# Kernel tuning notes

Measured on AMD Instinct MI355X. Metric: run time of the kernel, lower is better.

## Reference

```python
import jax, jax.numpy as jnp
import numpy as np
from jax import lax

EPS = 1e-6
CLAMP = 1e4


def _ln_last(x, w, b):
    # fp32 LayerNorm over last dim
    mu = jnp.mean(x, axis=-1, keepdims=True)
    var = jnp.mean(jnp.square(x - mu), axis=-1, keepdims=True)
    return (x - mu) * lax.rsqrt(var + EPS) * w + b


def _nan_clean(x):
    return jnp.nan_to_num(x, nan=0.0, posinf=CLAMP, neginf=-CLAMP)


def setup_inputs() -> dict:
    key = jax.random.key(0)
    B, C, H, W = 4, 256, 64, 64
    hid = 2 * C  # expand=2
    k = 3        # d_conv
    ks = jax.random.split(key, 12)
    s = 0.02
    return {
        "x": jax.random.normal(ks[0], (B, C, H, W), jnp.float32),
        "ln2d_w": jnp.ones((C,), jnp.float32),
        "ln2d_b": jnp.zeros((C,), jnp.float32),
        "inproj_w": jax.random.normal(ks[1], (C, C), jnp.float32) * s,
        "inproj_b": jnp.zeros((C,), jnp.float32),
        "dw2d_w": jax.random.normal(ks[2], (C, 3, 3), jnp.float32) * s,
        "dw2d_b": jnp.zeros((C,), jnp.float32),
        "ssm_ln_w": jnp.ones((C,), jnp.float32),
        "ssm_ln_b": jnp.zeros((C,), jnp.float32),
        "ssm_in_w": jax.random.normal(ks[3], (2 * hid, C), jnp.float32) * s,
        "ssm_in_b": jnp.zeros((2 * hid,), jnp.float32),
        "ssm_dw_w": jax.random.normal(ks[4], (hid, k), jnp.float32) * s,
        "ssm_dw_b": jnp.zeros((hid,), jnp.float32),
        "ssm_out_w": jax.random.normal(ks[5], (C, hid), jnp.float32) * s,
        "ssm_out_b": jnp.zeros((C,), jnp.float32),
        "outproj_w": jax.random.normal(ks[6], (C, C), jnp.float32) * s,
        "outproj_b": jnp.zeros((C,), jnp.float32),
    }


def reference(x, ln2d_w, ln2d_b, inproj_w, inproj_b, dw2d_w, dw2d_b,
              ssm_ln_w, ssm_ln_b, ssm_in_w, ssm_in_b, ssm_dw_w, ssm_dw_b,
              ssm_out_w, ssm_out_b, outproj_w, outproj_b):
    B, C, H, W = x.shape
    L = H * W

    # LN2d over channel dim (per-pixel LN on C)
    y = _ln_last(x.transpose(0, 2, 3, 1), ln2d_w, ln2d_b).transpose(0, 3, 1, 2)

    # 1x1 conv in_proj
    y = jnp.einsum('bchw,oc->bohw', y, inproj_w) + inproj_b[None, :, None, None]

    # depthwise 3x3 conv, SAME padding
    y = lax.conv_general_dilated(
        y, dw2d_w[:, None, :, :], (1, 1), ((1, 1), (1, 1)),
        dimension_numbers=('NCHW', 'OIHW', 'NCHW'),
        feature_group_count=C) + dw2d_b[None, :, None, None]

    # cross-scan: 4 routes (B,L,C)
    s0 = y.reshape(B, C, L).transpose(0, 2, 1)                      # row-major
    s1 = s0[:, ::-1]                                                # reversed
    s2 = y.transpose(0, 1, 3, 2).reshape(B, C, L).transpose(0, 2, 1)  # col-major
    s3 = s2[:, ::-1]
    s = jnp.concatenate([s0, s1, s2, s3], axis=0)  # (4B, L, C), shared SSM weights

    # MambaOrLite fallback: LN -> GLU -> depthwise conv1d -> out proj + residual
    r = _ln_last(s, ssm_ln_w, ssm_ln_b)
    r = r @ ssm_in_w.T + ssm_in_b                   # (4B, L, 2*hid)
    a, g = jnp.split(r, 2, axis=-1)
    r = a * jax.nn.sigmoid(g)                       # (4B, L, hid)
    r = r.transpose(0, 2, 1)                        # (4B, hid, L)
    hid = r.shape[1]
    k = ssm_dw_w.shape[-1]
    pad = ((k - 1) // 2, k // 2)
    r = lax.conv_general_dilated(
        r, ssm_dw_w[:, None, :], (1,), (pad,),
        dimension_numbers=('NCH', 'OIH', 'NCH'),
        feature_group_count=hid) + ssm_dw_b[None, :, None]
    r = r.transpose(0, 2, 1) @ ssm_out_w.T + ssm_out_b  # (4B, L, C)
    ys = _nan_clean(r) + s

    # cross-merge: average the 4 routes back to (B,C,H,W)
    y0, y1, y2, y3 = jnp.split(ys, 4, axis=0)
    m0 = y0.transpose(0, 2, 1).reshape(B, C, H, W)
    m1 = y1[:, ::-1].transpose(0, 2, 1).reshape(B, C, H, W)
    m2 = y2.transpose(0, 2, 1).reshape(B, C, W, H).transpose(0, 1, 3, 2)
    m3 = y3[:, ::-1].transpose(0, 2, 1).reshape(B, C, W, H).transpose(0, 1, 3, 2)
    m = (m0 + m1 + m2 + m3) * 0.25

    out = jnp.einsum('bchw,oc->bohw', m, outproj_w) + outproj_b[None, :, None, None]
    out = _nan_clean(out)
    return out + x
```

## Files before the change

### kernel.cpp

```cpp
#include <hip/hip_runtime.h>

typedef float f32x4 __attribute__((ext_vector_type(4)));
typedef __bf16 bf16x8 __attribute__((ext_vector_type(8)));
typedef unsigned short u16;
typedef unsigned int u32;

__device__ __forceinline__ float bf2f(u32 bits16) {
  u32 x = (bits16 & 0xffffu) << 16;
  return __builtin_bit_cast(float, x);
}
__device__ __forceinline__ u16 f2bf(float f) {
  u32 x = __builtin_bit_cast(u32, f);
  x += 0x7fffu + ((x >> 16) & 1u);
  return (u16)(x >> 16);
}
__device__ __forceinline__ void gload16(const void* g, void* l) {
  __builtin_amdgcn_global_load_lds((__attribute__((address_space(1))) void*)g,
                                   (__attribute__((address_space(3))) void*)l,
                                   16, 0, 0);
}

__global__ __launch_bounds__(256) void k_tobf16(const float* __restrict__ s,
                                                u16* __restrict__ d, int n) {
  int i = (blockIdx.x * 256 + threadIdx.x) * 4;
  if (i + 3 < n) {
    float4 v = *(const float4*)&s[i];
    u32 a = (u32)f2bf(v.x) | ((u32)f2bf(v.y) << 16);
    u32 b = (u32)f2bf(v.z) | ((u32)f2bf(v.w) << 16);
    *(uint2*)&d[i] = make_uint2(a, b);
  }
}

__global__ __launch_bounds__(256) void k_cvec(const float* __restrict__ Wout,
                                              const float* __restrict__ dwb,
                                              const float* __restrict__ outb,
                                              float* __restrict__ cvec) {
  int o = threadIdx.x;
  float s = outb[o];
  for (int k = 0; k < 512; ++k) s += dwb[k] * Wout[o * 512 + k];
  cvec[o] = s;
}

__global__ __launch_bounds__(256) void k_dwT(const float* __restrict__ dww,
                                             float* __restrict__ wT) {
  int c = threadIdx.x;
  #pragma unroll
  for (int j = 0; j < 9; ++j) wT[j * 256 + c] = dww[c * 9 + j];
}

__global__ __launch_bounds__(512) void k_scanw(const float* __restrict__ dww,
                                               float* __restrict__ w02,
                                               float* __restrict__ w14) {
  int c = threadIdx.x;
  w02[c] = dww[c * 3 + 0] + dww[c * 3 + 2];
  w14[c] = 4.f * dww[c * 3 + 1];
}

__global__ __launch_bounds__(256)
void k_ln2d(const float* __restrict__ x, const float* __restrict__ lw,
            const float* __restrict__ lb, u16* __restrict__ A) {
  __shared__ float ps1[4][64], ps2[4][64];
  __shared__ float mu[64], rsd[64];
  __shared__ float T[64 * 67];
  int tid = threadIdx.x;
  int wv = tid >> 6, p = tid & 63;
  int n0 = blockIdx.x * 64;
  int bb = n0 >> 12;
  int hw0 = n0 & 4095;
  const float* xb = x + ((size_t)bb << 20);
  float s1 = 0.f, s2 = 0.f;
  for (int i = 0; i < 64; ++i) {
    int c = wv * 64 + i;
    float v = xb[((size_t)c << 12) + hw0 + p];
    s1 += v; s2 += v * v;
  }
  ps1[wv][p] = s1; ps2[wv][p] = s2;
  __syncthreads();
  if (tid < 64) {
    float S1 = ps1[0][tid] + ps1[1][tid] + ps1[2][tid] + ps1[3][tid];
    float S2 = ps2[0][tid] + ps2[1][tid] + ps2[2][tid] + ps2[3][tid];
    float m = S1 * (1.f / 256.f);
    float var = S2 * (1.f / 256.f) - m * m;
    mu[tid] = m;
    rsd[tid] = rsqrtf(var + 1e-6f);
  }
  __syncthreads();
  for (int cc = 0; cc < 4; ++cc) {
    #pragma unroll
    for (int i = 0; i < 16; ++i) {
      int cl = i * 4 + wv;
      int c = cc * 64 + cl;
      float v = xb[((size_t)c << 12) + hw0 + p];
      T[cl * 67 + p] = (v - mu[p]) * rsd[p] * lw[c] + lb[c];
    }
    __syncthreads();
    int p2b = tid >> 4, c4 = (tid & 15) * 4;
    #pragma unroll
    for (int i2 = 0; i2 < 4; ++i2) {
      int p2 = p2b + 16 * i2;
      u32 a = (u32)f2bf(T[(c4 + 0) * 67 + p2]) | ((u32)f2bf(T[(c4 + 1) * 67 + p2]) << 16);
      u32 b = (u32)f2bf(T[(c4 + 2) * 67 + p2]) | ((u32)f2bf(T[(c4 + 3) * 67 + p2]) << 16);
      *(uint2*)&A[(size_t)(n0 + p2) * 256 + cc * 64 + c4] = make_uint2(a, b);
    }
    __syncthreads();
  }
}

__global__ __launch_bounds__(256)
void k_dw3x3_ln(const u16* __restrict__ Y1, const float* __restrict__ wT,
                const float* __restrict__ dwb, const float* __restrict__ lnw,
                const float* __restrict__ lnb, u16* __restrict__ Yc,
                u16* __restrict__ A) {
  int tid = threadIdx.x;
  int n = blockIdx.x * 4 + (tid >> 6);
  int lane = tid & 63;
  int c0 = lane * 4;
  int b = n >> 12, hw = n & 4095, h = hw >> 6, w = hw & 63;
  float4 b4 = *(const float4*)&dwb[c0];
  float a0 = b4.x, a1 = b4.y, a2 = b4.z, a3 = b4.w;
  #pragma unroll
  for (int ky = 0; ky < 3; ++ky) {
    int hh = h + ky - 1;
    if (hh < 0 || hh > 63) continue;
    #pragma unroll
    for (int kx = 0; kx < 3; ++kx) {
      int ww = w + kx - 1;
      if (ww < 0 || ww > 63) continue;
      size_t nn = ((size_t)b << 12) + (hh << 6) + ww;
      uint2 u = *(const uint2*)&Y1[nn * 256 + c0];
      float4 w4 = *(const float4*)&wT[(ky * 3 + kx) * 256 + c0];
      a0 += bf2f(u.x) * w4.x;
      a1 += bf2f(u.x >> 16) * w4.y;
      a2 += bf2f(u.y) * w4.z;
      a3 += bf2f(u.y >> 16) * w4.w;
    }
  }
  u32 p0 = (u32)f2bf(a0) | ((u32)f2bf(a1) << 16);
  u32 p1 = (u32)f2bf(a2) | ((u32)f2bf(a3) << 16);
  *(uint2*)&Yc[(size_t)n * 256 + c0] = make_uint2(p0, p1);
  float s1 = a0 + a1 + a2 + a3;
  float s2 = a0 * a0 + a1 * a1 + a2 * a2 + a3 * a3;
  #pragma unroll
  for (int off = 1; off < 64; off <<= 1) {
    s1 += __shfl_xor(s1, off);
    s2 += __shfl_xor(s2, off);
  }
  float m = s1 * (1.f / 256.f);
  float var = s2 * (1.f / 256.f) - m * m;
  float rs = rsqrtf(var + 1e-6f);
  float4 w4 = *(const float4*)&lnw[c0];
  float4 g4 = *(const float4*)&lnb[c0];
  float o0 = (a0 - m) * rs * w4.x + g4.x;
  float o1 = (a1 - m) * rs * w4.y + g4.y;
  float o2 = (a2 - m) * rs * w4.z + g4.z;
  float o3 = (a3 - m) * rs * w4.w + g4.w;
  u32 q0 = (u32)f2bf(o0) | ((u32)f2bf(o1) << 16);
  u32 q1 = (u32)f2bf(o2) | ((u32)f2bf(o3) << 16);
  *(uint2*)&A[(size_t)n * 256 + c0] = make_uint2(q0, q1);
}

__global__ __launch_bounds__(256)
void k_scan(const u16* __restrict__ G, const float* __restrict__ w02,
            const float* __restrict__ w14, u16* __restrict__ Z) {
  int tid = threadIdx.x;
  int n = blockIdx.x * 2 + (tid >> 7);
  int c0 = (tid & 127) * 4;
  int b = n >> 12, hw = n & 4095, h = hw >> 6, w = hw & 63;
  int m = w * 64 + h;
  float s0 = 0.f, s1 = 0.f, s2 = 0.f, s3 = 0.f;
  auto addn = [&](int nn) {
    uint2 u = *(const uint2*)&G[(size_t)nn * 512 + c0];
    s0 += bf2f(u.x); s1 += bf2f(u.x >> 16);
    s2 += bf2f(u.y); s3 += bf2f(u.y >> 16);
  };
  if (hw > 0) addn(n - 1);
  if (hw < 4095) addn(n + 1);
  if (m > 0)   { int mm = m - 1; addn((b << 12) + ((mm & 63) << 6) + (mm >> 6)); }
  if (m < 4095){ int mm = m + 1; addn((b << 12) + ((mm & 63) << 6) + (mm >> 6)); }
  uint2 uc = *(const uint2*)&G[(size_t)n * 512 + c0];
  float g0 = bf2f(uc.x), g1 = bf2f(uc.x >> 16), g2 = bf2f(uc.y), g3 = bf2f(uc.y >> 16);
  float4 wa = *(const float4*)&w02[c0];
  float4 wb = *(const float4*)&w14[c0];
  float z0 = wa.x * s0 + wb.x * g0;
  float z1 = wa.y * s1 + wb.y * g1;
  float z2 = wa.z * s2 + wb.z * g2;
  float z3 = wa.w * s3 + wb.w * g3;
  u32 p0 = (u32)f2bf(z0) | ((u32)f2bf(z1) << 16);
  u32 p1 = (u32)f2bf(z2) | ((u32)f2bf(z3) << 16);
  *(uint2*)&Z[(size_t)n * 512 + c0] = make_uint2(p0, p1);
}

template <int EPI>
__global__ __launch_bounds__(256, 2)
void k_gemm(const u16* __restrict__ A, const u16* __restrict__ W,
            const float* __restrict__ bias, int K, int nTo, int ldo,
            u16* __restrict__ outb, const u16* __restrict__ resb,
            float* __restrict__ outf, const float* __restrict__ resf) {
  __shared__ u16 tA[128 * 32];
  __shared__ u16 tW[128 * 32];
  int tid = threadIdx.x;
  int tn = blockIdx.x / nTo, to = blockIdx.x % nTo;
  int n0 = tn * 128, o0 = to * 128;
  int lane = tid & 63, wv = tid >> 6;
  int wr = wv >> 1, wc = wv & 1;
  int fr = lane & 15, kc = lane >> 4;
  int srow = lane >> 2, scol = (lane & 3) * 8;
  f32x4 acc[4][4] = {};
  int nK = K >> 5;
  for (int kt = 0; kt < nK; ++kt) {
    int k0 = kt * 32;
    #pragma unroll
    for (int pass = 0; pass < 2; ++pass) {
      int rowblk = wv * 32 + pass * 16;
      gload16(A + (size_t)(n0 + rowblk + srow) * K + k0 + scol, &tA[rowblk * 32]);
      gload16(W + (size_t)(o0 + rowblk + srow) * K + k0 + scol, &tW[rowblk * 32]);
    }
    __syncthreads();
    const u16* fa = (EPI == 2) ? tW : tA;
    const u16* fb = (EPI == 2) ? tA : tW;
    bf16x8 af[4], wf[4];
    #pragma unroll
    for (int m = 0; m < 4; ++m)
      af[m] = *(const bf16x8*)&fa[(wr * 64 + m * 16 + fr) * 32 + kc * 8];
    #pragma unroll
    for (int n = 0; n < 4; ++n)
      wf[n] = *(const bf16x8*)&fb[(wc * 64 + n * 16 + fr) * 32 + kc * 8];
    #pragma unroll
    for (int m = 0; m < 4; ++m)
      #pragma unroll
      for (int n = 0; n < 4; ++n)
        acc[m][n] = __builtin_amdgcn_mfma_f32_16x16x32_bf16(af[m], wf[n], acc[m][n], 0, 0, 0);
    __syncthreads();
  }
  #pragma unroll
  for (int m = 0; m < 4; ++m) {
    #pragma unroll
    for (int n = 0; n < 4; ++n) {
      #pragma unroll
      for (int r = 0; r < 4; ++r) {
        float v = acc[m][n][r];
        if (EPI == 0) {
          int gn = n0 + wr * 64 + m * 16 + kc * 4 + r;
          int go = o0 + wc * 64 + n * 16 + fr;
          outb[(size_t)gn * ldo + go] = f2bf(v + bias[go]);
        } else if (EPI == 1) {
          int gn = n0 + wr * 64 + m * 16 + kc * 4 + r;
          int go = o0 + wc * 64 + n * 16 + fr;
          float val = 0.25f * v + bias[go] + bf2f(resb[(size_t)gn * 256 + go]);
          outb[(size_t)gn * 256 + go] = f2bf(val);
        } else {
          int go = o0 + wr * 64 + m * 16 + kc * 4 + r;
          int gn = n0 + wc * 64 + n * 16 + fr;
          int b = gn >> 12, hw = gn & 4095;
          size_t idx = (((size_t)(b * 256 + go)) << 12) + hw;
          outf[idx] = v + bias[go] + resf[idx];
        }
      }
    }
  }
}

__global__ __launch_bounds__(256, 2)
void k_gemm_gate(const u16* __restrict__ A, const u16* __restrict__ W,
                 const float* __restrict__ bias, u16* __restrict__ G) {
  __shared__ u16 tA[128 * 32];
  __shared__ u16 tWa[128 * 32];
  __shared__ u16 tWg[128 * 32];
  int tid = threadIdx.x;
  int tn = blockIdx.x >> 2, to = blockIdx.x & 3;
  int n0 = tn * 128, o0 = to * 128;
  int lane = tid & 63, wv = tid >> 6;
  int wr = wv >> 1, wc = wv & 1;
  int fr = lane & 15, kc = lane >> 4;
  int srow = lane >> 2, scol = (lane & 3) * 8;
  const int K = 256;
  f32x4 acca[4][4] = {}, accg[4][4] = {};
  for (int kt = 0; kt < 8; ++kt) {
    int k0 = kt * 32;
    #pragma unroll
    for (int pass = 0; pass < 2; ++pass) {
      int rowblk = wv * 32 + pass * 16;
      gload16(A + (size_t)(n0 + rowblk + srow) * K + k0 + scol, &tA[rowblk * 32]);
      gload16(W + (size_t)(o0 + rowblk + srow) * K + k0 + scol, &tWa[rowblk * 32]);
      gload16(W + (size_t)(512 + o0 + rowblk + srow) * K + k0 + scol, &tWg[rowblk * 32]);
    }
    __syncthreads();
    bf16x8 af[4];
    #pragma unroll
    for (int m = 0; m < 4; ++m)
      af[m] = *(const bf16x8*)&tA[(wr * 64 + m * 16 + fr) * 32 + kc * 8];
    #pragma unroll
    for (int n = 0; n < 4; ++n) {
      bf16x8 wfa = *(const bf16x8*)&tWa[(wc * 64 + n * 16 + fr) * 32 + kc * 8];
      #pragma unroll
      for (int m = 0; m < 4; ++m)
        acca[m][n] = __builtin_amdgcn_mfma_f32_16x16x32_bf16(af[m], wfa, acca[m][n], 0, 0, 0);
      bf16x8 wfg = *(const bf16x8*)&tWg[(wc * 64 + n * 16 + fr) * 32 + kc * 8];
      #pragma unroll
      for (int m = 0; m < 4; ++m)
        accg[m][n] = __builtin_amdgcn_mfma_f32_16x16x32_bf16(af[m], wfg, accg[m][n], 0, 0, 0);
    }
    __syncthreads();
  }
  #pragma unroll
  for (int m = 0; m < 4; ++m) {
    #pragma unroll
    for (int n = 0; n < 4; ++n) {
      #pragma unroll
      for (int r = 0; r < 4; ++r) {
        int gn = n0 + wr * 64 + m * 16 + kc * 4 + r;
        int go = o0 + wc * 64 + n * 16 + fr;
        float a = acca[m][n][r] + bias[go];
        float g = accg[m][n][r] + bias[512 + go];
        float val = a / (1.f + expf(-g));
        G[(size_t)gn * 512 + go] = f2bf(val);
      }
    }
  }
}

extern "C" void kernel_launch(void* const* d_in, const int* in_sizes, int n_in,
                              void* d_out, int out_size, void* d_ws, size_t ws_size,
                              hipStream_t stream) {
  const float* x         = (const float*)d_in[0];
  const float* ln2d_w    = (const float*)d_in[1];
  const float* ln2d_b    = (const float*)d_in[2];
  const float* inproj_w  = (const float*)d_in[3];
  const float* inproj_b  = (const float*)d_in[4];
  const float* dw2d_w    = (const float*)d_in[5];
  const float* dw2d_b    = (const float*)d_in[6];
  const float* ssm_ln_w  = (const float*)d_in[7];
  const float* ssm_ln_b  = (const float*)d_in[8];
  const float* ssm_in_w  = (const float*)d_in[9];
  const float* ssm_in_b  = (const float*)d_in[10];
  const float* ssm_dw_w  = (const float*)d_in[11];
  const float* ssm_dw_b  = (const float*)d_in[12];
  const float* ssm_out_w = (const float*)d_in[13];
  const float* ssm_out_b = (const float*)d_in[14];
  const float* outproj_w = (const float*)d_in[15];
  const float* outproj_b = (const float*)d_in[16];
  float* out = (float*)d_out;

  char* ws = (char*)d_ws;
  size_t off = 0;
  auto take = [&](size_t bytes) -> char* {
    char* p = ws + off;
    off = (off + bytes + 255) & ~(size_t)255;
    return p;
  };
  u16* w1b   = (u16*)take(65536 * 2);
  u16* w2b   = (u16*)take(262144 * 2);
  u16* w3b   = (u16*)take(131072 * 2);
  u16* w4b   = (u16*)take(65536 * 2);
  float* cvec= (float*)take(256 * 4);
  float* wT9 = (float*)take(9 * 256 * 4);
  float* w02 = (float*)take(512 * 4);
  float* w14 = (float*)take(512 * 4);
  u16* Abuf  = (u16*)take((size_t)16384 * 256 * 2);
  u16* Y1    = (u16*)take((size_t)16384 * 256 * 2);
  u16* Yc    = (u16*)take((size_t)16384 * 256 * 2);
  u16* G     = (u16*)take((size_t)16384 * 512 * 2);
  u16* Z     = (u16*)take((size_t)16384 * 512 * 2);
  (void)ws_size; (void)in_sizes; (void)n_in; (void)out_size;

  k_tobf16<<<64, 256, 0, stream>>>(inproj_w, w1b, 65536);
  k_tobf16<<<256, 256, 0, stream>>>(ssm_in_w, w2b, 262144);
  k_tobf16<<<128, 256, 0, stream>>>(ssm_out_w, w3b, 131072);
  k_tobf16<<<64, 256, 0, stream>>>(outproj_w, w4b, 65536);
  k_cvec<<<1, 256, 0, stream>>>(ssm_out_w, ssm_dw_b, ssm_out_b, cvec);
  k_dwT<<<1, 256, 0, stream>>>(dw2d_w, wT9);
  k_scanw<<<1, 512, 0, stream>>>(ssm_dw_w, w02, w14);

  k_ln2d<<<256, 256, 0, stream>>>(x, ln2d_w, ln2d_b, Abuf);
  k_gemm<0><<<256, 256, 0, stream>>>(Abuf, w1b, inproj_b, 256, 2, 256, Y1, nullptr, nullptr, nullptr);
  k_dw3x3_ln<<<4096, 256, 0, stream>>>(Y1, wT9, dw2d_b, ssm_ln_w, ssm_ln_b, Yc, Abuf);
  k_gemm_gate<<<512, 256, 0, stream>>>(Abuf, w2b, ssm_in_b, G);
  k_scan<<<8192, 256, 0, stream>>>(G, w02, w14, Z);
  k_gemm<1><<<256, 256, 0, stream>>>(Z, w3b, cvec, 512, 2, 256, Abuf, Yc, nullptr, nullptr);
  k_gemm<2><<<256, 256, 0, stream>>>(Abuf, w4b, outproj_b, 256, 2, 256, nullptr, nullptr, out, x);
}
```

Before: 130.8 us.

## Double-buffer GEMMs with smaller tiles, fuse prep kernels, single-pass LN2d

```diff
diff --git a/kernel.cpp b/kernel.cpp
--- a/kernel.cpp
+++ b/kernel.cpp
@@ -5,8 +5,8 @@
 typedef unsigned short u16;
 typedef unsigned int u32;
 
-__device__ __forceinline__ float bf2f(u32 bits16) {
-  u32 x = (bits16 & 0xffffu) << 16;
+__device__ __forceinline__ float bf2f(u32 b) {
+  u32 x = (b & 0xffffu) << 16;
   return __builtin_bit_cast(float, x);
 }
 __device__ __forceinline__ u16 f2bf(float f) {
@@ -20,61 +20,76 @@
                                    16, 0, 0);
 }
 
-__global__ __launch_bounds__(256) void k_tobf16(const float* __restrict__ s,
-                                                u16* __restrict__ d, int n) {
-  int i = (blockIdx.x * 256 + threadIdx.x) * 4;
-  if (i + 3 < n) {
+__global__ __launch_bounds__(256)
+void k_prep(const float* __restrict__ inproj_w, const float* __restrict__ ssm_in_w,
+            const float* __restrict__ ssm_out_w, const float* __restrict__ outproj_w,
+            const float* __restrict__ dw2d_w, const float* __restrict__ ssm_dw_w,
+            const float* __restrict__ ssm_dw_b, const float* __restrict__ ssm_out_b,
+            u16* __restrict__ w1b, u16* __restrict__ w2b, u16* __restrict__ w3b,
+            u16* __restrict__ w4b, float* __restrict__ cvec, float* __restrict__ wT9,
+            float* __restrict__ w02, float* __restrict__ w14) {
+  int bid = blockIdx.x, tid = threadIdx.x;
+  if (bid < 512) {
+    const float* s; u16* d; int base;
+    if (bid < 256)      { s = ssm_in_w;  d = w2b; base = bid; }
+    else if (bid < 384) { s = ssm_out_w; d = w3b; base = bid - 256; }
+    else if (bid < 448) { s = inproj_w;  d = w1b; base = bid - 384; }
+    else                { s = outproj_w; d = w4b; base = bid - 448; }
+    int i = base * 1024 + tid * 4;
     float4 v = *(const float4*)&s[i];
     u32 a = (u32)f2bf(v.x) | ((u32)f2bf(v.y) << 16);
     u32 b = (u32)f2bf(v.z) | ((u32)f2bf(v.w) << 16);
     *(uint2*)&d[i] = make_uint2(a, b);
-  }
-}
-
-__global__ __launch_bounds__(256) void k_cvec(const float* __restrict__ Wout,
-                                              const float* __restrict__ dwb,
-                                              const float* __restrict__ outb,
-                                              float* __restrict__ cvec) {
-  int o = threadIdx.x;
-  float s = outb[o];
-  for (int k = 0; k < 512; ++k) s += dwb[k] * Wout[o * 512 + k];
-  cvec[o] = s;
-}
-
-__global__ __launch_bounds__(256) void k_dwT(const float* __restrict__ dww,
-                                             float* __restrict__ wT) {
-  int c = threadIdx.x;
-  #pragma unroll
-  for (int j = 0; j < 9; ++j) wT[j * 256 + c] = dww[c * 9 + j];
-}
-
-__global__ __launch_bounds__(512) void k_scanw(const float* __restrict__ dww,
-                                               float* __restrict__ w02,
-                                               float* __restrict__ w14) {
-  int c = threadIdx.x;
-  w02[c] = dww[c * 3 + 0] + dww[c * 3 + 2];
-  w14[c] = 4.f * dww[c * 3 + 1];
-}
-
-__global__ __launch_bounds__(256)
+  } else if (bid == 512) {
+    float s = ssm_out_b[tid];
+    const float* wr = ssm_out_w + (size_t)tid * 512;
+    #pragma unroll 8
+    for (int k = 0; k < 512; ++k) s += ssm_dw_b[k] * wr[k];
+    cvec[tid] = s;
+  } else {
+    #pragma unroll
+    for (int j = 0; j < 9; ++j) wT9[j * 256 + tid] = dw2d_w[tid * 9 + j];
+    #pragma unroll
+    for (int q = 0; q < 2; ++q) {
+      int c = tid + q * 256;
+      w02[c] = ssm_dw_w[c * 3 + 0] + ssm_dw_w[c * 3 + 2];
+      w14[c] = 4.f * ssm_dw_w[c * 3 + 1];
+    }
+  }
+}
+
+__global__ __launch_bounds__(256, 2)
 void k_ln2d(const float* __restrict__ x, const float* __restrict__ lw,
             const float* __restrict__ lb, u16* __restrict__ A) {
+  __shared__ float T[256 * 65];
   __shared__ float ps1[4][64], ps2[4][64];
   __shared__ float mu[64], rsd[64];
-  __shared__ float T[64 * 67];
-  int tid = threadIdx.x;
-  int wv = tid >> 6, p = tid & 63;
-  int n0 = blockIdx.x * 64;
-  int bb = n0 >> 12;
-  int hw0 = n0 & 4095;
+  int tid = threadIdx.x, wv = tid >> 6, lane = tid & 63;
+  int cq = lane >> 4, p4 = (lane & 15) * 4;
+  int n0 = blockIdx.x * 64, bb = n0 >> 12, hw0 = n0 & 4095;
   const float* xb = x + ((size_t)bb << 20);
-  float s1 = 0.f, s2 = 0.f;
-  for (int i = 0; i < 64; ++i) {
-    int c = wv * 64 + i;
-    float v = xb[((size_t)c << 12) + hw0 + p];
-    s1 += v; s2 += v * v;
-  }
-  ps1[wv][p] = s1; ps2[wv][p] = s2;
+  float s0 = 0, s1 = 0, s2 = 0, s3 = 0;
+  float q0 = 0, q1 = 0, q2 = 0, q3 = 0;
+  #pragma unroll 4
+  for (int i = 0; i < 16; ++i) {
+    int c = wv * 64 + i * 4 + cq;
+    float4 v = *(const float4*)&xb[((size_t)c << 12) + hw0 + p4];
+    T[c * 65 + p4 + 0] = v.x; T[c * 65 + p4 + 1] = v.y;
+    T[c * 65 + p4 + 2] = v.z; T[c * 65 + p4 + 3] = v.w;
+    s0 += v.x; s1 += v.y; s2 += v.z; s3 += v.w;
+    q0 += v.x * v.x; q1 += v.y * v.y; q2 += v.z * v.z; q3 += v.w * v.w;
+  }
+  #pragma unroll
+  for (int off = 16; off < 64; off <<= 1) {
+    s0 += __shfl_xor(s0, off); s1 += __shfl_xor(s1, off);
+    s2 += __shfl_xor(s2, off); s3 += __shfl_xor(s3, off);
+    q0 += __shfl_xor(q0, off); q1 += __shfl_xor(q1, off);
+    q2 += __shfl_xor(q2, off); q3 += __shfl_xor(q3, off);
+  }
+  if (cq == 0) {
+    ps1[wv][p4 + 0] = s0; ps1[wv][p4 + 1] = s1; ps1[wv][p4 + 2] = s2; ps1[wv][p4 + 3] = s3;
+    ps2[wv][p4 + 0] = q0; ps2[wv][p4 + 1] = q1; ps2[wv][p4 + 2] = q2; ps2[wv][p4 + 3] = q3;
+  }
   __syncthreads();
   if (tid < 64) {
     float S1 = ps1[0][tid] + ps1[1][tid] + ps1[2][tid] + ps1[3][tid];
@@ -85,24 +100,24 @@
     rsd[tid] = rsqrtf(var + 1e-6f);
   }
   __syncthreads();
+  int c4b = (tid & 15) * 4, p2b = tid >> 4;
+  #pragma unroll
   for (int cc = 0; cc < 4; ++cc) {
-    #pragma unroll
-    for (int i = 0; i < 16; ++i) {
-      int cl = i * 4 + wv;
-      int c = cc * 64 + cl;
-      float v = xb[((size_t)c << 12) + hw0 + p];
-      T[cl * 67 + p] = (v - mu[p]) * rsd[p] * lw[c] + lb[c];
-    }
-    __syncthreads();
-    int p2b = tid >> 4, c4 = (tid & 15) * 4;
+    int c4 = cc * 64 + c4b;
+    float4 w4 = *(const float4*)&lw[c4];
+    float4 g4 = *(const float4*)&lb[c4];
     #pragma unroll
     for (int i2 = 0; i2 < 4; ++i2) {
       int p2 = p2b + 16 * i2;
-      u32 a = (u32)f2bf(T[(c4 + 0) * 67 + p2]) | ((u32)f2bf(T[(c4 + 1) * 67 + p2]) << 16);
-      u32 b = (u32)f2bf(T[(c4 + 2) * 67 + p2]) | ((u32)f2bf(T[(c4 + 3) * 67 + p2]) << 16);
-      *(uint2*)&A[(size_t)(n0 + p2) * 256 + cc * 64 + c4] = make_uint2(a, b);
-    }
-    __syncthreads();
+      float m = mu[p2], rs = rsd[p2];
+      float o0 = (T[(c4 + 0) * 65 + p2] - m) * rs * w4.x + g4.x;
+      float o1 = (T[(c4 + 1) * 65 + p2] - m) * rs * w4.y + g4.y;
+      float o2 = (T[(c4 + 2) * 65 + p2] - m) * rs * w4.z + g4.z;
+      float o3 = (T[(c4 + 3) * 65 + p2] - m) * rs * w4.w + g4.w;
+      u32 a = (u32)f2bf(o0) | ((u32)f2bf(o1) << 16);
+      u32 b = (u32)f2bf(o2) | ((u32)f2bf(o3) << 16);
+      *(uint2*)&A[(size_t)(n0 + p2) * 256 + c4] = make_uint2(a, b);
+    }
   }
 }
 
@@ -154,9 +169,9 @@
   float o1 = (a1 - m) * rs * w4.y + g4.y;
   float o2 = (a2 - m) * rs * w4.z + g4.z;
   float o3 = (a3 - m) * rs * w4.w + g4.w;
-  u32 q0 = (u32)f2bf(o0) | ((u32)f2bf(o1) << 16);
-  u32 q1 = (u32)f2bf(o2) | ((u32)f2bf(o3) << 16);
-  *(uint2*)&A[(size_t)n * 256 + c0] = make_uint2(q0, q1);
+  u32 qa = (u32)f2bf(o0) | ((u32)f2bf(o1) << 16);
+  u32 qb = (u32)f2bf(o2) | ((u32)f2bf(o3) << 16);
+  *(uint2*)&A[(size_t)n * 256 + c0] = make_uint2(qa, qb);
 }
 
 __global__ __launch_bounds__(256)
@@ -175,8 +190,8 @@
   };
   if (hw > 0) addn(n - 1);
   if (hw < 4095) addn(n + 1);
-  if (m > 0)   { int mm = m - 1; addn((b << 12) + ((mm & 63) << 6) + (mm >> 6)); }
-  if (m < 4095){ int mm = m + 1; addn((b << 12) + ((mm & 63) << 6) + (mm >> 6)); }
+  if (m > 0)    { int mm = m - 1; addn((b << 12) + ((mm & 63) << 6) + (mm >> 6)); }
+  if (m < 4095) { int mm = m + 1; addn((b << 12) + ((mm & 63) << 6) + (mm >> 6)); }
   uint2 uc = *(const uint2*)&G[(size_t)n * 512 + c0];
   float g0 = bf2f(uc.x), g1 = bf2f(uc.x >> 16), g2 = bf2f(uc.y), g3 = bf2f(uc.y >> 16);
   float4 wa = *(const float4*)&w02[c0];
@@ -191,66 +206,73 @@
 }
 
 template <int EPI>
-__global__ __launch_bounds__(256, 2)
-void k_gemm(const u16* __restrict__ A, const u16* __restrict__ W,
-            const float* __restrict__ bias, int K, int nTo, int ldo,
-            u16* __restrict__ outb, const u16* __restrict__ resb,
-            float* __restrict__ outf, const float* __restrict__ resf) {
-  __shared__ u16 tA[128 * 32];
-  __shared__ u16 tW[128 * 32];
-  int tid = threadIdx.x;
-  int tn = blockIdx.x / nTo, to = blockIdx.x % nTo;
-  int n0 = tn * 128, o0 = to * 128;
-  int lane = tid & 63, wv = tid >> 6;
-  int wr = wv >> 1, wc = wv & 1;
+__global__ __launch_bounds__(256, 4)
+void k_gemm2(const u16* __restrict__ R, const u16* __restrict__ Cm,
+             const float* __restrict__ bias, int K, int nCt, int ldo,
+             u16* __restrict__ outb, const u16* __restrict__ resb,
+             float* __restrict__ outf, const float* __restrict__ resf) {
+  __shared__ u16 tR[2][64 * 32];
+  __shared__ u16 tC[2][128 * 32];
+  int tid = threadIdx.x, lane = tid & 63, wv = tid >> 6;
+  int rt = blockIdx.x / nCt, ct = blockIdx.x % nCt;
+  int r0 = rt * 64, c0 = ct * 128;
   int fr = lane & 15, kc = lane >> 4;
-  int srow = lane >> 2, scol = (lane & 3) * 8;
-  f32x4 acc[4][4] = {};
+  int sr = lane >> 2, sc = (lane & 3) * 8;
+  f32x4 acc[4][2] = {};
   int nK = K >> 5;
-  for (int kt = 0; kt < nK; ++kt) {
+  const u16* gR  = R  + (size_t)(r0 + wv * 16 + sr) * K + sc;
+  const u16* gC0 = Cm + (size_t)(c0 + wv * 32 + sr) * K + sc;
+  const u16* gC1 = Cm + (size_t)(c0 + wv * 32 + 16 + sr) * K + sc;
+  auto STAGE = [&](int buf, int kt) {
     int k0 = kt * 32;
-    #pragma unroll
-    for (int pass = 0; pass < 2; ++pass) {
-      int rowblk = wv * 32 + pass * 16;
-      gload16(A + (size_t)(n0 + rowblk + srow) * K + k0 + scol, &tA[rowblk * 32]);
-      gload16(W + (size_t)(o0 + rowblk + srow) * K + k0 + scol, &tW[rowblk * 32]);
-    }
-    __syncthreads();
-    const u16* fa = (EPI == 2) ? tW : tA;
-    const u16* fb = (EPI == 2) ? tA : tW;
-    bf16x8 af[4], wf[4];
+    gload16(gR + k0,  &tR[buf][wv * 16 * 32]);
+    gload16(gC0 + k0, &tC[buf][(wv * 32) * 32]);
+    gload16(gC1 + k0, &tC[buf][(wv * 32 + 16) * 32]);
+  };
+  auto COMPUTE = [&](int buf) {
+    bf16x8 af[4], wf[2];
     #pragma unroll
     for (int m = 0; m < 4; ++m)
-      af[m] = *(const bf16x8*)&fa[(wr * 64 + m * 16 + fr) * 32 + kc * 8];
-    #pragma unroll
-    for (int n = 0; n < 4; ++n)
-      wf[n] = *(const bf16x8*)&fb[(wc * 64 + n * 16 + fr) * 32 + kc * 8];
+      af[m] = *(const bf16x8*)&tR[buf][(m * 16 + fr) * 32 + kc * 8];
+    #pragma unroll
+    for (int n = 0; n < 2; ++n)
+      wf[n] = *(const bf16x8*)&tC[buf][(wv * 32 + n * 16 + fr) * 32 + kc * 8];
     #pragma unroll
     for (int m = 0; m < 4; ++m)
       #pragma unroll
-      for (int n = 0; n < 4; ++n)
+      for (int n = 0; n < 2; ++n)
         acc[m][n] = __builtin_amdgcn_mfma_f32_16x16x32_bf16(af[m], wf[n], acc[m][n], 0, 0, 0);
+  };
+  STAGE(0, 0);
+  __syncthreads();
+  int cur = 0;
+  for (int kt = 0; kt < nK - 1; ++kt) {
+    STAGE(cur ^ 1, kt + 1);
+    __builtin_amdgcn_sched_barrier(0);
+    COMPUTE(cur);
     __syncthreads();
-  }
+    cur ^= 1;
+  }
+  COMPUTE(cur);
   #pragma unroll
   for (int m = 0; m < 4; ++m) {
     #pragma unroll
-    for (int n = 0; n < 4; ++n) {
+    for (int n = 0; n < 2; ++n) {
       #pragma unroll
       for (int r = 0; r < 4; ++r) {
         float v = acc[m][n][r];
         if (EPI == 0) {
-          int gn = n0 + wr * 64 + m * 16 + kc * 4 + r;
-          int go = o0 + wc * 64 + n * 16 + fr;
+          int gn = r0 + m * 16 + kc * 4 + r;
+          int go = c0 + wv * 32 + n * 16 + fr;
           outb[(size_t)gn * ldo + go] = f2bf(v + bias[go]);
         } else if (EPI == 1) {
-          int gn = n0 + wr * 64 + m * 16 + kc * 4 + r;
-          int go = o0 + wc * 64 + n * 16 + fr;
-          float val = 0.25f * v + bias[go] + bf2f(resb[(size_t)gn * 256 + go]);
-          outb[(size_t)gn * 256 + go] = f2bf(val);
+          int gn = r0 + m * 16 + kc * 4 + r;
+          int go = c0 + wv * 32 + n * 16 + fr;
+          outb[(size_t)gn * 256 + go] =
+              f2bf(0.25f * v + bias[go] + bf2f(resb[(size_t)gn * 256 + go]));
         } else {
-          int go = o0 + wr * 64 + m * 16 + kc * 4 + r;
-          int gn = n0 + wc * 64 + n * 16 + fr;
+          int go = r0 + m * 16 + kc * 4 + r;
+          int gn = c0 + wv * 32 + n * 16 + fr;
           int b = gn >> 12, hw = gn & 4095;
           size_t idx = (((size_t)(b * 256 + go)) << 12) + hw;
           outf[idx] = v + bias[go] + resf[idx];
@@ -260,60 +282,72 @@
   }
 }
 
-__global__ __launch_bounds__(256, 2)
-void k_gemm_gate(const u16* __restrict__ A, const u16* __restrict__ W,
-                 const float* __restrict__ bias, u16* __restrict__ G) {
-  __shared__ u16 tA[128 * 32];
-  __shared__ u16 tWa[128 * 32];
-  __shared__ u16 tWg[128 * 32];
-  int tid = threadIdx.x;
-  int tn = blockIdx.x >> 2, to = blockIdx.x & 3;
-  int n0 = tn * 128, o0 = to * 128;
-  int lane = tid & 63, wv = tid >> 6;
-  int wr = wv >> 1, wc = wv & 1;
+__global__ __launch_bounds__(256, 3)
+void k_gate2(const u16* __restrict__ A, const u16* __restrict__ W,
+             const float* __restrict__ bias, u16* __restrict__ G) {
+  __shared__ u16 tR[2][64 * 32];
+  __shared__ u16 tCa[2][128 * 32];
+  __shared__ u16 tCg[2][128 * 32];
+  int tid = threadIdx.x, lane = tid & 63, wv = tid >> 6;
+  int rt = blockIdx.x >> 2, ot = blockIdx.x & 3;
+  int r0 = rt * 64, o0 = ot * 128;
   int fr = lane & 15, kc = lane >> 4;
-  int srow = lane >> 2, scol = (lane & 3) * 8;
+  int sr = lane >> 2, sc = (lane & 3) * 8;
   const int K = 256;
-  f32x4 acca[4][4] = {}, accg[4][4] = {};
-  for (int kt = 0; kt < 8; ++kt) {
+  f32x4 acca[4][2] = {}, accg[4][2] = {};
+  const u16* gR  = A + (size_t)(r0 + wv * 16 + sr) * K + sc;
+  const u16* gA0 = W + (size_t)(o0 + wv * 32 + sr) * K + sc;
+  const u16* gA1 = W + (size_t)(o0 + wv * 32 + 16 + sr) * K + sc;
+  const u16* gG0 = W + (size_t)(512 + o0 + wv * 32 + sr) * K + sc;
+  const u16* gG1 = W + (size_t)(512 + o0 + wv * 32 + 16 + sr) * K + sc;
+  auto STAGE = [&](int buf, int kt) {
     int k0 = kt * 32;
-    #pragma unroll
-    for (int pass = 0; pass < 2; ++pass) {
-      int rowblk = wv * 32 + pass * 16;
-      gload16(A + (size_t)(n0 + rowblk + srow) * K + k0 + scol, &tA[rowblk * 32]);
-      gload16(W + (size_t)(o0 + rowblk + srow) * K + k0 + scol, &tWa[rowblk * 32]);
-      gload16(W + (size_t)(512 + o0 + rowblk + srow) * K + k0 + scol, &tWg[rowblk * 32]);
-    }
+    gload16(gR + k0,  &tR[buf][wv * 16 * 32]);
+    gload16(gA0 + k0, &tCa[buf][(wv * 32) * 32]);
+    gload16(gA1 + k0, &tCa[buf][(wv * 32 + 16) * 32]);
+    gload16(gG0 + k0, &tCg[buf][(wv * 32) * 32]);
+    gload16(gG1 + k0, &tCg[buf][(wv * 32 + 16) * 32]);
+  };
+  auto COMPUTE = [&](int buf) {
+    bf16x8 af[4], wa[2], wg[2];
+    #pragma unroll
+    for (int m = 0; m < 4; ++m)
+      af[m] = *(const bf16x8*)&tR[buf][(m * 16 + fr) * 32 + kc * 8];
+    #pragma unroll
+    for (int n = 0; n < 2; ++n) {
+      wa[n] = *(const bf16x8*)&tCa[buf][(wv * 32 + n * 16 + fr) * 32 + kc * 8];
+      wg[n] = *(const bf16x8*)&tCg[buf][(wv * 32 + n * 16 + fr) * 32 + kc * 8];
+    }
+    #pragma unroll
+    for (int m = 0; m < 4; ++m)
+      #pragma unroll
+      for (int n = 0; n < 2; ++n) {
+        acca[m][n] = __builtin_amdgcn_mfma_f32_16x16x32_bf16(af[m], wa[n], acca[m][n], 0, 0, 0);
+        accg[m][n] = __builtin_amdgcn_mfma_f32_16x16x32_bf16(af[m], wg[n], accg[m][n], 0, 0, 0);
+      }
+  };
+  STAGE(0, 0);
+  __syncthreads();
+  int cur = 0;
+  for (int kt = 0; kt < 7; ++kt) {
+    STAGE(cur ^ 1, kt + 1);
+    __builtin_amdgcn_sched_barrier(0);
+    COMPUTE(cur);
     __syncthreads();
-    bf16x8 af[4];
-    #pragma unroll
-    for (int m = 0; m < 4; ++m)
-      af[m] = *(const bf16x8*)&tA[(wr * 64 + m * 16 + fr) * 32 + kc * 8];
-    #pragma unroll
-    for (int n = 0; n < 4; ++n) {
-      bf16x8 wfa = *(const bf16x8*)&tWa[(wc * 64 + n * 16 + fr) * 32 + kc * 8];
-      #pragma unroll
-      for (int m = 0; m < 4; ++m)
-        acca[m][n] = __builtin_amdgcn_mfma_f32_16x16x32_bf16(af[m], wfa, acca[m][n], 0, 0, 0);
-      bf16x8 wfg = *(const bf16x8*)&tWg[(wc * 64 + n * 16 + fr) * 32 + kc * 8];
-      #pragma unroll
-      for (int m = 0; m < 4; ++m)
-        accg[m][n] = __builtin_amdgcn_mfma_f32_16x16x32_bf16(af[m], wfg, accg[m][n], 0, 0, 0);
-    }
-    __syncthreads();
-  }
+    cur ^= 1;
+  }
+  COMPUTE(cur);
   #pragma unroll
   for (int m = 0; m < 4; ++m) {
     #pragma unroll
-    for (int n = 0; n < 4; ++n) {
+    for (int n = 0; n < 2; ++n) {
       #pragma unroll
       for (int r = 0; r < 4; ++r) {
-        int gn = n0 + wr * 64 + m * 16 + kc * 4 + r;
-        int go = o0 + wc * 64 + n * 16 + fr;
+        int gn = r0 + m * 16 + kc * 4 + r;
+        int go = o0 + wv * 32 + n * 16 + fr;
         float a = acca[m][n][r] + bias[go];
         float g = accg[m][n][r] + bias[512 + go];
-        float val = a / (1.f + expf(-g));
-        G[(size_t)gn * 512 + go] = f2bf(val);
+        G[(size_t)gn * 512 + go] = f2bf(a / (1.f + expf(-g)));
       }
     }
   }
@@ -348,34 +382,32 @@
     off = (off + bytes + 255) & ~(size_t)255;
     return p;
   };
-  u16* w1b   = (u16*)take(65536 * 2);
-  u16* w2b   = (u16*)take(262144 * 2);
-  u16* w3b   = (u16*)take(131072 * 2);
-  u16* w4b   = (u16*)take(65536 * 2);
-  float* cvec= (float*)take(256 * 4);
-  float* wT9 = (float*)take(9 * 256 * 4);
-  float* w02 = (float*)take(512 * 4);
-  float* w14 = (float*)take(512 * 4);
-  u16* Abuf  = (u16*)take((size_t)16384 * 256 * 2);
-  u16* Y1    = (u16*)take((size_t)16384 * 256 * 2);
-  u16* Yc    = (u16*)take((size_t)16384 * 256 * 2);
-  u16* G     = (u16*)take((size_t)16384 * 512 * 2);
-  u16* Z     = (u16*)take((size_t)16384 * 512 * 2);
+  u16* w1b    = (u16*)take(65536 * 2);
+  u16* w2b    = (u16*)take(262144 * 2);
+  u16* w3b    = (u16*)take(131072 * 2);
+  u16* w4b    = (u16*)take(65536 * 2);
+  float* cvec = (float*)take(256 * 4);
+  float* wT9  = (float*)take(9 * 256 * 4);
+  float* w02  = (float*)take(512 * 4);
+  float* w14  = (float*)take(512 * 4);
+  u16* Abuf   = (u16*)take((size_t)16384 * 256 * 2);
+  u16* Y1     = (u16*)take((size_t)16384 * 256 * 2);
+  u16* Yc     = (u16*)take((size_t)16384 * 256 * 2);
+  u16* G      = (u16*)take((size_t)16384 * 512 * 2);
+  u16* Z      = (u16*)take((size_t)16384 * 512 * 2);
   (void)ws_size; (void)in_sizes; (void)n_in; (void)out_size;
 
-  k_tobf16<<<64, 256, 0, stream>>>(inproj_w, w1b, 65536);
-  k_tobf16<<<256, 256, 0, stream>>>(ssm_in_w, w2b, 262144);
-  k_tobf16<<<128, 256, 0, stream>>>(ssm_out_w, w3b, 131072);
-  k_tobf16<<<64, 256, 0, stream>>>(outproj_w, w4b, 65536);
-  k_cvec<<<1, 256, 0, stream>>>(ssm_out_w, ssm_dw_b, ssm_out_b, cvec);
-  k_dwT<<<1, 256, 0, stream>>>(dw2d_w, wT9);
-  k_scanw<<<1, 512, 0, stream>>>(ssm_dw_w, w02, w14);
-
+  k_prep<<<514, 256, 0, stream>>>(inproj_w, ssm_in_w, ssm_out_w, outproj_w,
+                                  dw2d_w, ssm_dw_w, ssm_dw_b, ssm_out_b,
+                                  w1b, w2b, w3b, w4b, cvec, wT9, w02, w14);
   k_ln2d<<<256, 256, 0, stream>>>(x, ln2d_w, ln2d_b, Abuf);
-  k_gemm<0><<<256, 256, 0, stream>>>(Abuf, w1b, inproj_b, 256, 2, 256, Y1, nullptr, nullptr, nullptr);
+  k_gemm2<0><<<512, 256, 0, stream>>>(Abuf, w1b, inproj_b, 256, 2, 256,
+                                      Y1, nullptr, nullptr, nullptr);
   k_dw3x3_ln<<<4096, 256, 0, stream>>>(Y1, wT9, dw2d_b, ssm_ln_w, ssm_ln_b, Yc, Abuf);
-  k_gemm_gate<<<512, 256, 0, stream>>>(Abuf, w2b, ssm_in_b, G);
+  k_gate2<<<1024, 256, 0, stream>>>(Abuf, w2b, ssm_in_b, G);
   k_scan<<<8192, 256, 0, stream>>>(G, w02, w14, Z);
-  k_gemm<1><<<256, 256, 0, stream>>>(Z, w3b, cvec, 512, 2, 256, Abuf, Yc, nullptr, nullptr);
-  k_gemm<2><<<256, 256, 0, stream>>>(Abuf, w4b, outproj_b, 256, 2, 256, nullptr, nullptr, out, x);
-}
+  k_gemm2<1><<<512, 256, 0, stream>>>(Z, w3b, cvec, 512, 2, 256,
+                                      Abuf, Yc, nullptr, nullptr);
+  k_gemm2<2><<<512, 256, 0, stream>>>(w4b, Abuf, outproj_b, 256, 128, 0,
+                                      nullptr, nullptr, out, x);
+}
```

Measured after the change: 113.0 us. -13.6%, faster.
